# Kernel tuning notes

Hardware: AMD Instinct MI355X
Metric: run time of the kernel (lower is better)

Reference implementation:

```python
import jax, jax.numpy as jnp
import numpy as np

INPUT_DIM = 512
HIDDEN_DIM = 512
B, N = 8, 2048


def setup_inputs() -> dict:
    key = jax.random.key(0)
    ks = jax.random.split(key, 9)
    s_in = 1.0 / np.sqrt(INPUT_DIM)
    s_h = 1.0 / np.sqrt(HIDDEN_DIM)
    return {
        "X": jax.random.normal(ks[0], (B, N, INPUT_DIM), dtype=jnp.float32),
        "Wq": jax.random.uniform(ks[1], (INPUT_DIM, HIDDEN_DIM), minval=-s_in, maxval=s_in),
        "bq": jnp.zeros((HIDDEN_DIM,), jnp.float32),
        "Wk": jax.random.uniform(ks[2], (INPUT_DIM, HIDDEN_DIM), minval=-s_in, maxval=s_in),
        "bk": jnp.zeros((HIDDEN_DIM,), jnp.float32),
        "Wv": jax.random.uniform(ks[3], (INPUT_DIM, HIDDEN_DIM), minval=-s_in, maxval=s_in),
        "bv": jnp.zeros((HIDDEN_DIM,), jnp.float32),
        "Wo": jax.random.uniform(ks[4], (HIDDEN_DIM, INPUT_DIM), minval=-s_h, maxval=s_h),
        "bo": jnp.zeros((INPUT_DIM,), jnp.float32),
        "ln_gamma": jnp.ones((INPUT_DIM,), jnp.float32),
        "ln_beta": jnp.zeros((INPUT_DIM,), jnp.float32),
    }


def reference(X, Wq, bq, Wk, bk, Wv, bv, Wo, bo, ln_gamma, ln_beta):
    q = X @ Wq + bq                      # [B,N,H]
    k = X @ Wk + bk
    v = X @ Wv + bv
    scores = jnp.einsum('bnh,bmh->bnm', q, k) / jnp.sqrt(jnp.float32(HIDDEN_DIM))
    attn = jax.nn.softmax(scores, axis=-1)      # [B,N,N]
    ctx = jnp.einsum('bnm,bmh->bnh', attn, v)   # [B,N,H]
    out = ctx @ Wo + bo + X                      # residual
    mu = jnp.mean(out, axis=-1, keepdims=True)
    var = jnp.var(out, axis=-1, keepdims=True)
    normed = (out - mu) / jnp.sqrt(var + 1e-5)
    return normed * ln_gamma + ln_beta
```

## Files before the change

### kernel.cpp

```cpp
#include <hip/hip_runtime.h>
#include <cstdint>
#include <cstddef>


typedef __bf16 bf16x8 __attribute__((ext_vector_type(8)));
typedef float  f32x4  __attribute__((ext_vector_type(4)));

__device__ __forceinline__ uint16_t f2bf(float f) {
  union { float f; uint32_t u; } v; v.f = f;
  uint32_t r = v.u + 0x7FFFu + ((v.u >> 16) & 1u);
  return (uint16_t)(r >> 16);
}

__device__ __forceinline__ void gld16(const uint16_t* g, uint16_t* l) {
  __builtin_amdgcn_global_load_lds(
      (__attribute__((address_space(1))) void*)(g),
      (__attribute__((address_space(3))) void*)(l), 16, 0, 0);
}

template <int MODE, int BM, int BN, int WM, int WN>
__global__ __launch_bounds__(512, 4) void gemm_k(
    const uint16_t* __restrict__ A, const uint16_t* __restrict__ Bt,
    void* __restrict__ OutA, uint16_t* __restrict__ OutK,
    uint16_t* __restrict__ OutVT, float* __restrict__ rsum, int K, int lda,
    int ldb, const float* __restrict__ b0, const float* __restrict__ b1,
    const float* __restrict__ b2, const float* __restrict__ Xres, float scale) {
  constexpr int MT = (BM / WM) / 16;
  constexpr int NT = (BN / WN) / 16;
  static_assert(MT == 4 && NT == 4, "wave tile must be 64x64");
  constexpr int AI = (BM >= 128) ? BM / 128 : 1;
  constexpr int BI = BN / 128;
  constexpr int PW = AI + BI;
  __shared__ alignas(16) uint16_t As[3][BM * 32];
  __shared__ alignas(16) uint16_t Bs[3][BN * 32];

  const int tid = threadIdx.x;
  const int w = tid >> 6, lane = tid & 63;
  const int wm = w / WN, wn = w % WN;

  const int gx = gridDim.x, gy = gridDim.y;
  const int nwg = gx * gy * gridDim.z;
  const int hw = blockIdx.x + gx * (blockIdx.y + gy * blockIdx.z);
  const int lg = (hw & 7) * (nwg >> 3) + (hw >> 3);
  const int bx = lg % gx, byz = lg / gx;
  const int by = byz % gy, z = byz / gy;

  const int m0 = by * BM, n0 = bx * BN;

  const uint16_t* Ab = A;
  const uint16_t* Bb = Bt;
  if (MODE == 1) { Ab += (size_t)z * 2048 * 512;  Bb += (size_t)z * 2048 * 512; }
  if (MODE == 2) { Ab += (size_t)z * 2048 * 2048; Bb += (size_t)z * 512 * 2048; }

  const int kc = (((lane & 3) ^ ((lane >> 2) & 3) ^ (lane >> 4)) * 8);
  const int rbA = (BM >= 128) ? w * (BM / 8) : (w & 3) * 16;
  const int rbB = w * (BN / 8);
  const uint16_t* gA = Ab + (size_t)(m0 + rbA + (lane >> 2)) * lda + kc;
  const uint16_t* gB = Bb + (size_t)(n0 + rbB + (lane >> 2)) * ldb + kc;

  f32x4 acc[MT][NT];
#pragma unroll
  for (int i = 0; i < MT; i++)
#pragma unroll
    for (int j = 0; j < NT; j++) acc[i][j] = (f32x4){0.f, 0.f, 0.f, 0.f};

  const int lr = lane & 15, q4 = lane >> 4;
  const int swz = (((lane >> 4) ^ (lr & 3) ^ (lr >> 2)) * 8);
  const int iters = K >> 5;

  auto stage = [&](int t, int buf) {
    const int k0 = t * 32;
#pragma unroll
    for (int j = 0; j < AI; j++)
      gld16(gA + k0 + (size_t)(j * 16) * lda, &As[buf][(rbA + j * 16) * 32]);
#pragma unroll
    for (int j = 0; j < BI; j++)
      gld16(gB + k0 + (size_t)(j * 16) * ldb, &Bs[buf][(rbB + j * 16) * 32]);
  };

  auto compute = [&](int buf) {
    bf16x8 af[MT], bfr[NT];
#pragma unroll
    for (int t = 0; t < MT; t++)
      af[t] = *(const bf16x8*)&As[buf][(wm * (BM / WM) + t * 16 + lr) * 32 + swz];
#pragma unroll
    for (int t = 0; t < NT; t++)
      bfr[t] = *(const bf16x8*)&Bs[buf][(wn * (BN / WN) + t * 16 + lr) * 32 + swz];
#pragma unroll
    for (int nt = 0; nt < NT; nt++)
#pragma unroll
      for (int mt = 0; mt < MT; mt++)
        acc[mt][nt] = __builtin_amdgcn_mfma_f32_16x16x32_bf16(
            af[mt], bfr[nt], acc[mt][nt], 0, 0, 0);
  };

  stage(0, 0);
  stage(1, 1);
  int buf = 0;
  for (int i = 0; i < iters - 1; ++i) {
    asm volatile("s_waitcnt vmcnt(%0)" ::"i"(PW) : "memory");
    __builtin_amdgcn_s_barrier();
    if (i + 2 < iters) stage(i + 2, (buf + 2 >= 3) ? buf - 1 : buf + 2);
    compute(buf);
    buf = (buf == 2) ? 0 : buf + 1;
  }
  asm volatile("s_waitcnt vmcnt(0)" ::: "memory");
  __builtin_amdgcn_s_barrier();
  compute(buf);

  if (MODE == 1) {
    uint16_t* Sp = (uint16_t*)OutA + (size_t)z * 2048 * 2048;
#pragma unroll
    for (int mt = 0; mt < MT; mt++) {
      float rp[4] = {0.f, 0.f, 0.f, 0.f};
#pragma unroll
      for (int nt = 0; nt < NT; nt++) {
#pragma unroll
        for (int i = 0; i < 4; i++) {
          const int row = m0 + wm * (BM / WM) + mt * 16 + q4 * 4 + i;
          const int col = n0 + wn * (BN / WN) + nt * 16 + lr;
          const float e = __expf(acc[mt][nt][i] * scale);
          Sp[(size_t)row * 2048 + col] = f2bf(e);
          rp[i] += e;
        }
      }
#pragma unroll
      for (int i = 0; i < 4; i++) {
        float p = rp[i];
        p += __shfl_xor(p, 1); p += __shfl_xor(p, 2);
        p += __shfl_xor(p, 4); p += __shfl_xor(p, 8);
        if (lr == 0) {
          const int row = m0 + wm * (BM / WM) + mt * 16 + q4 * 4 + i;
          atomicAdd(&rsum[z * 2048 + row], p);
        }
      }
    }
  } else if (MODE == 2) {
#pragma unroll
    for (int mt = 0; mt < MT; mt++) {
#pragma unroll
      for (int i = 0; i < 4; i++) {
        const int row = m0 + wm * (BM / WM) + mt * 16 + q4 * 4 + i;
        const float sc = 1.0f / rsum[z * 2048 + row];
#pragma unroll
        for (int nt = 0; nt < NT; nt++) {
          const int col = n0 + wn * (BN / WN) + nt * 16 + lr;
          ((uint16_t*)OutA)[((size_t)z * 2048 + row) * 512 + col] =
              f2bf(acc[mt][nt][i] * sc);
        }
      }
    }
  } else if (MODE == 4) {
    __shared__ float redS[8][64];
    __shared__ float redQ[8][64];
    float* Op = (float*)OutA;
    __syncthreads();
#pragma unroll
    for (int mt = 0; mt < MT; mt++) {
#pragma unroll
      for (int i = 0; i < 4; i++) {
        const int rl = mt * 16 + q4 * 4 + i;
        const int row = m0 + rl;
        float ps = 0.f, pq = 0.f;
#pragma unroll
        for (int nt = 0; nt < NT; nt++) {
          const int col = wn * 64 + nt * 16 + lr;
          float v = acc[mt][nt][i] + b0[col] + Xres[(size_t)row * 512 + col];
          acc[mt][nt][i] = v;
          ps += v; pq += v * v;
        }
        ps += __shfl_xor(ps, 1); pq += __shfl_xor(pq, 1);
        ps += __shfl_xor(ps, 2); pq += __shfl_xor(pq, 2);
        ps += __shfl_xor(ps, 4); pq += __shfl_xor(pq, 4);
        ps += __shfl_xor(ps, 8); pq += __shfl_xor(pq, 8);
        if (lr == 0) { redS[w][rl] = ps; redQ[w][rl] = pq; }
      }
    }
    __syncthreads();
#pragma unroll
    for (int mt = 0; mt < MT; mt++) {
#pragma unroll
      for (int i = 0; i < 4; i++) {
        const int rl = mt * 16 + q4 * 4 + i;
        const int row = m0 + rl;
        float s8 = 0.f, q8 = 0.f;
#pragma unroll
        for (int ww = 0; ww < 8; ww++) { s8 += redS[ww][rl]; q8 += redQ[ww][rl]; }
        const float mean = s8 * (1.f / 512.f);
        const float var = q8 * (1.f / 512.f) - mean * mean;
        const float rstd = rsqrtf(var + 1e-5f);
#pragma unroll
        for (int nt = 0; nt < NT; nt++) {
          const int col = wn * 64 + nt * 16 + lr;
          Op[(size_t)row * 512 + col] =
              (acc[mt][nt][i] - mean) * rstd * b1[col] + b2[col];
        }
      }
    }
  } else {
#pragma unroll
    for (int mt = 0; mt < MT; mt++) {
#pragma unroll
      for (int nt = 0; nt < NT; nt++) {
#pragma unroll
        for (int i = 0; i < 4; i++) {
          const int row = m0 + wm * (BM / WM) + mt * 16 + q4 * 4 + i;
          const int col = n0 + wn * (BN / WN) + nt * 16 + lr;
          const float v = acc[mt][nt][i];
          const int which = col >> 9, c = col & 511;
          if (which == 0) {
            ((uint16_t*)OutA)[(size_t)row * 512 + c] = f2bf(v + b0[c]);
          } else if (which == 1) {
            OutK[(size_t)row * 512 + c] = f2bf(v + b1[c]);
          } else {
            OutVT[(size_t)(row >> 11) * (512 * 2048) + (size_t)c * 2048 +
                  (row & 2047)] = f2bf(v + b2[c]);
          }
        }
      }
    }
  }
}

__global__ __launch_bounds__(256) void cvt_all_k(
    const float* __restrict__ X, uint16_t* __restrict__ Xb,
    const float* __restrict__ Wq, const float* __restrict__ Wk,
    const float* __restrict__ Wv, const float* __restrict__ Wo,
    uint16_t* __restrict__ Wt, float* __restrict__ rsum) {
  const int i = blockIdx.x * 256 + threadIdx.x;
  const float4 f = ((const float4*)X)[i];
  uint32_t lo = (uint32_t)f2bf(f.x) | ((uint32_t)f2bf(f.y) << 16);
  uint32_t hi = (uint32_t)f2bf(f.z) | ((uint32_t)f2bf(f.w) << 16);
  ((uint2*)Xb)[i] = make_uint2(lo, hi);
  if (i < 16384) rsum[i] = 0.f;
  if (i < 2048 * 512) {
    const int n = i >> 9, kk = i & 511;
    const int which = n >> 9, c = n & 511;
    const float* W =
        (which == 0) ? Wq : (which == 1) ? Wk : (which == 2) ? Wv : Wo;
    Wt[i] = f2bf(W[kk * 512 + c]);
  }
}

extern "C" void kernel_launch(void* const* d_in, const int* in_sizes, int n_in,
                              void* d_out, int out_size, void* d_ws,
                              size_t ws_size, hipStream_t stream) {
  const float* X     = (const float*)d_in[0];
  const float* Wq    = (const float*)d_in[1];
  const float* bq    = (const float*)d_in[2];
  const float* Wk    = (const float*)d_in[3];
  const float* bk    = (const float*)d_in[4];
  const float* Wv    = (const float*)d_in[5];
  const float* bv    = (const float*)d_in[6];
  const float* Wo    = (const float*)d_in[7];
  const float* bo    = (const float*)d_in[8];
  const float* gamma = (const float*)d_in[9];
  const float* beta  = (const float*)d_in[10];
  float* out = (float*)d_out;

  char* ws = (char*)d_ws;
  uint16_t* S    = (uint16_t*)(ws);
  uint16_t* Xb   = (uint16_t*)(ws);
  uint16_t* Wt   = (uint16_t*)(ws + 67108864);
  uint16_t* q    = (uint16_t*)(ws + 69206016);
  uint16_t* kb   = (uint16_t*)(ws + 85983232);
  uint16_t* vT   = (uint16_t*)(ws + 102760448);
  float*    rsum = (float*)(ws + 119537664);
  uint16_t* ctx  = q;

  cvt_all_k<<<dim3(8192), dim3(256), 0, stream>>>(X, Xb, Wq, Wk, Wv, Wo, Wt,
                                                  rsum);
  gemm_k<0, 256, 128, 4, 2><<<dim3(12, 64, 1), dim3(512), 0, stream>>>(
      Xb, Wt, (void*)q, kb, vT, nullptr, 512, 512, 512, bq, bk, bv, nullptr,
      1.f);
  gemm_k<1, 256, 128, 4, 2><<<dim3(16, 8, 8), dim3(512), 0, stream>>>(
      q, kb, (void*)S, nullptr, nullptr, rsum, 512, 512, 512, nullptr, nullptr,
      nullptr, nullptr, 0.044194173824159216f);
  gemm_k<2, 256, 128, 4, 2><<<dim3(4, 8, 8), dim3(512), 0, stream>>>(
      S, vT, (void*)ctx, nullptr, nullptr, rsum, 2048, 2048, 2048, nullptr,
      nullptr, nullptr, nullptr, 1.f);
  gemm_k<4, 64, 512, 1, 8><<<dim3(1, 256, 1), dim3(512), 0, stream>>>(
      ctx, Wt + 1536 * 512, (void*)out, nullptr, nullptr, nullptr, 512, 512,
      512, bo, gamma, beta, X, 1.f);
}
```

Measured before the change: 316.8 us.

## Add BK=64 double-buffered GEMM kernel with 256-wide tiles for QKV/attention

```diff
diff --git a/kernel.cpp b/kernel.cpp
--- a/kernel.cpp
+++ b/kernel.cpp
@@ -18,25 +18,24 @@
       (__attribute__((address_space(3))) void*)(l), 16, 0, 0);
 }
 
-template <int MODE, int BM, int BN, int WM, int WN>
-__global__ __launch_bounds__(512, 4) void gemm_k(
+template <int MODE, int BM, int BN>
+__global__ __launch_bounds__(512, 2) void gemm2_k(
     const uint16_t* __restrict__ A, const uint16_t* __restrict__ Bt,
     void* __restrict__ OutA, uint16_t* __restrict__ OutK,
     uint16_t* __restrict__ OutVT, float* __restrict__ rsum, int K, int lda,
     int ldb, const float* __restrict__ b0, const float* __restrict__ b1,
-    const float* __restrict__ b2, const float* __restrict__ Xres, float scale) {
-  constexpr int MT = (BM / WM) / 16;
-  constexpr int NT = (BN / WN) / 16;
-  static_assert(MT == 4 && NT == 4, "wave tile must be 64x64");
-  constexpr int AI = (BM >= 128) ? BM / 128 : 1;
-  constexpr int BI = BN / 128;
-  constexpr int PW = AI + BI;
-  __shared__ alignas(16) uint16_t As[3][BM * 32];
-  __shared__ alignas(16) uint16_t Bs[3][BN * 32];
+    const float* __restrict__ b2, float scale) {
+  constexpr int MT = (BM / 2) / 16;
+  constexpr int NT = (BN / 4) / 16;
+  constexpr int AI = BM / 64;
+  constexpr int BI = BN / 64;
+  static_assert(NT == 4, "BN must be 256");
+  __shared__ alignas(16) uint16_t As[2][BM * 64];
+  __shared__ alignas(16) uint16_t Bs[2][BN * 64];
 
   const int tid = threadIdx.x;
   const int w = tid >> 6, lane = tid & 63;
-  const int wm = w / WN, wn = w % WN;
+  const int wm = w >> 2, wn = w & 3;
 
   const int gx = gridDim.x, gy = gridDim.y;
   const int nwg = gx * gy * gridDim.z;
@@ -52,11 +51,22 @@
   if (MODE == 1) { Ab += (size_t)z * 2048 * 512;  Bb += (size_t)z * 2048 * 512; }
   if (MODE == 2) { Ab += (size_t)z * 2048 * 2048; Bb += (size_t)z * 512 * 2048; }
 
-  const int kc = (((lane & 3) ^ ((lane >> 2) & 3) ^ (lane >> 4)) * 8);
-  const int rbA = (BM >= 128) ? w * (BM / 8) : (w & 3) * 16;
-  const int rbB = w * (BN / 8);
-  const uint16_t* gA = Ab + (size_t)(m0 + rbA + (lane >> 2)) * lda + kc;
-  const uint16_t* gB = Bb + (size_t)(n0 + rbB + (lane >> 2)) * ldb + kc;
+  const int l3 = lane >> 3, l7 = lane & 7;
+  const int csw = (l7 ^ l3) * 8;
+  const uint16_t* gA = Ab + (size_t)(m0 + w * (BM / 8) + l3) * lda + csw;
+  const uint16_t* gB = Bb + (size_t)(n0 + w * (BN / 8) + l3) * ldb + csw;
+
+  auto stage = [&](int t, int b) {
+    const int k0 = t * 64;
+#pragma unroll
+    for (int j = 0; j < AI; j++)
+      gld16(gA + k0 + (size_t)(j * 8) * lda,
+            &As[b][(w * (BM / 8) + j * 8) * 64]);
+#pragma unroll
+    for (int j = 0; j < BI; j++)
+      gld16(gB + k0 + (size_t)(j * 8) * ldb,
+            &Bs[b][(w * (BN / 8) + j * 8) * 64]);
+  };
 
   f32x4 acc[MT][NT];
 #pragma unroll
@@ -65,48 +75,43 @@
     for (int j = 0; j < NT; j++) acc[i][j] = (f32x4){0.f, 0.f, 0.f, 0.f};
 
   const int lr = lane & 15, q4 = lane >> 4;
-  const int swz = (((lane >> 4) ^ (lr & 3) ^ (lr >> 2)) * 8);
-  const int iters = K >> 5;
-
-  auto stage = [&](int t, int buf) {
-    const int k0 = t * 32;
-#pragma unroll
-    for (int j = 0; j < AI; j++)
-      gld16(gA + k0 + (size_t)(j * 16) * lda, &As[buf][(rbA + j * 16) * 32]);
-#pragma unroll
-    for (int j = 0; j < BI; j++)
-      gld16(gB + k0 + (size_t)(j * 16) * ldb, &Bs[buf][(rbB + j * 16) * 32]);
-  };
-
-  auto compute = [&](int buf) {
-    bf16x8 af[MT], bfr[NT];
-#pragma unroll
-    for (int t = 0; t < MT; t++)
-      af[t] = *(const bf16x8*)&As[buf][(wm * (BM / WM) + t * 16 + lr) * 32 + swz];
-#pragma unroll
-    for (int t = 0; t < NT; t++)
-      bfr[t] = *(const bf16x8*)&Bs[buf][(wn * (BN / WN) + t * 16 + lr) * 32 + swz];
-#pragma unroll
-    for (int nt = 0; nt < NT; nt++)
-#pragma unroll
-      for (int mt = 0; mt < MT; mt++)
-        acc[mt][nt] = __builtin_amdgcn_mfma_f32_16x16x32_bf16(
-            af[mt], bfr[nt], acc[mt][nt], 0, 0, 0);
-  };
+  const int rc0 = ((q4) ^ (lr & 7)) * 8;
+  const int rc1 = ((4 + q4) ^ (lr & 7)) * 8;
+
+  const int NK = K >> 6;
 
   stage(0, 0);
-  stage(1, 1);
-  int buf = 0;
-  for (int i = 0; i < iters - 1; ++i) {
-    asm volatile("s_waitcnt vmcnt(%0)" ::"i"(PW) : "memory");
-    __builtin_amdgcn_s_barrier();
-    if (i + 2 < iters) stage(i + 2, (buf + 2 >= 3) ? buf - 1 : buf + 2);
-    compute(buf);
-    buf = (buf == 2) ? 0 : buf + 1;
-  }
   asm volatile("s_waitcnt vmcnt(0)" ::: "memory");
   __builtin_amdgcn_s_barrier();
-  compute(buf);
+
+  int cur = 0;
+  for (int t = 0; t < NK; ++t) {
+    if (t + 1 < NK) stage(t + 1, cur ^ 1);
+#pragma unroll
+    for (int ks = 0; ks < 2; ks++) {
+      const int rc = ks ? rc1 : rc0;
+      bf16x8 af[MT], bfr[NT];
+#pragma unroll
+      for (int mt = 0; mt < MT; mt++)
+        af[mt] = *(const bf16x8*)
+            &As[cur][(wm * (BM / 2) + mt * 16 + lr) * 64 + rc];
+#pragma unroll
+      for (int nt = 0; nt < NT; nt++)
+        bfr[nt] = *(const bf16x8*)&Bs[cur][(wn * 64 + nt * 16 + lr) * 64 + rc];
+#pragma unroll
+      for (int nt = 0; nt < NT; nt++)
+#pragma unroll
+        for (int mt = 0; mt < MT; mt++)
+          acc[mt][nt] = __builtin_amdgcn_mfma_f32_16x16x32_bf16(
+              af[mt], bfr[nt], acc[mt][nt], 0, 0, 0);
+    }
+    if (t + 1 < NK) {
+      asm volatile("s_waitcnt lgkmcnt(0)" ::: "memory");
+      asm volatile("s_waitcnt vmcnt(0)" ::: "memory");
+      __builtin_amdgcn_s_barrier();
+      cur ^= 1;
+    }
+  }
 
   if (MODE == 1) {
     uint16_t* Sp = (uint16_t*)OutA + (size_t)z * 2048 * 2048;
@@ -117,8 +122,8 @@
       for (int nt = 0; nt < NT; nt++) {
 #pragma unroll
         for (int i = 0; i < 4; i++) {
-          const int row = m0 + wm * (BM / WM) + mt * 16 + q4 * 4 + i;
-          const int col = n0 + wn * (BN / WN) + nt * 16 + lr;
+          const int row = m0 + wm * (BM / 2) + mt * 16 + q4 * 4 + i;
+          const int col = n0 + wn * 64 + nt * 16 + lr;
           const float e = __expf(acc[mt][nt][i] * scale);
           Sp[(size_t)row * 2048 + col] = f2bf(e);
           rp[i] += e;
@@ -130,7 +135,7 @@
         p += __shfl_xor(p, 1); p += __shfl_xor(p, 2);
         p += __shfl_xor(p, 4); p += __shfl_xor(p, 8);
         if (lr == 0) {
-          const int row = m0 + wm * (BM / WM) + mt * 16 + q4 * 4 + i;
+          const int row = m0 + wm * (BM / 2) + mt * 16 + q4 * 4 + i;
           atomicAdd(&rsum[z * 2048 + row], p);
         }
       }
@@ -140,72 +145,25 @@
     for (int mt = 0; mt < MT; mt++) {
 #pragma unroll
       for (int i = 0; i < 4; i++) {
-        const int row = m0 + wm * (BM / WM) + mt * 16 + q4 * 4 + i;
+        const int row = m0 + wm * (BM / 2) + mt * 16 + q4 * 4 + i;
         const float sc = 1.0f / rsum[z * 2048 + row];
 #pragma unroll
         for (int nt = 0; nt < NT; nt++) {
-          const int col = n0 + wn * (BN / WN) + nt * 16 + lr;
+          const int col = n0 + wn * 64 + nt * 16 + lr;
           ((uint16_t*)OutA)[((size_t)z * 2048 + row) * 512 + col] =
               f2bf(acc[mt][nt][i] * sc);
         }
       }
     }
-  } else if (MODE == 4) {
-    __shared__ float redS[8][64];
-    __shared__ float redQ[8][64];
-    float* Op = (float*)OutA;
-    __syncthreads();
+  } else {
 #pragma unroll
     for (int mt = 0; mt < MT; mt++) {
 #pragma unroll
-      for (int i = 0; i < 4; i++) {
-        const int rl = mt * 16 + q4 * 4 + i;
-        const int row = m0 + rl;
-        float ps = 0.f, pq = 0.f;
-#pragma unroll
-        for (int nt = 0; nt < NT; nt++) {
-          const int col = wn * 64 + nt * 16 + lr;
-          float v = acc[mt][nt][i] + b0[col] + Xres[(size_t)row * 512 + col];
-          acc[mt][nt][i] = v;
-          ps += v; pq += v * v;
-        }
-        ps += __shfl_xor(ps, 1); pq += __shfl_xor(pq, 1);
-        ps += __shfl_xor(ps, 2); pq += __shfl_xor(pq, 2);
-        ps += __shfl_xor(ps, 4); pq += __shfl_xor(pq, 4);
-        ps += __shfl_xor(ps, 8); pq += __shfl_xor(pq, 8);
-        if (lr == 0) { redS[w][rl] = ps; redQ[w][rl] = pq; }
-      }
-    }
-    __syncthreads();
-#pragma unroll
-    for (int mt = 0; mt < MT; mt++) {
-#pragma unroll
-      for (int i = 0; i < 4; i++) {
-        const int rl = mt * 16 + q4 * 4 + i;
-        const int row = m0 + rl;
-        float s8 = 0.f, q8 = 0.f;
-#pragma unroll
-        for (int ww = 0; ww < 8; ww++) { s8 += redS[ww][rl]; q8 += redQ[ww][rl]; }
-        const float mean = s8 * (1.f / 512.f);
-        const float var = q8 * (1.f / 512.f) - mean * mean;
-        const float rstd = rsqrtf(var + 1e-5f);
-#pragma unroll
-        for (int nt = 0; nt < NT; nt++) {
-          const int col = wn * 64 + nt * 16 + lr;
-          Op[(size_t)row * 512 + col] =
-              (acc[mt][nt][i] - mean) * rstd * b1[col] + b2[col];
-        }
-      }
-    }
-  } else {
-#pragma unroll
-    for (int mt = 0; mt < MT; mt++) {
-#pragma unroll
       for (int nt = 0; nt < NT; nt++) {
 #pragma unroll
         for (int i = 0; i < 4; i++) {
-          const int row = m0 + wm * (BM / WM) + mt * 16 + q4 * 4 + i;
-          const int col = n0 + wn * (BN / WN) + nt * 16 + lr;
+          const int row = m0 + wm * (BM / 2) + mt * 16 + q4 * 4 + i;
+          const int col = n0 + wn * 64 + nt * 16 + lr;
           const float v = acc[mt][nt][i];
           const int which = col >> 9, c = col & 511;
           if (which == 0) {
@@ -217,6 +175,141 @@
                   (row & 2047)] = f2bf(v + b2[c]);
           }
         }
+      }
+    }
+  }
+}
+
+template <int MODE, int BM, int BN, int WM, int WN>
+__global__ __launch_bounds__(512, 4) void gemm_k(
+    const uint16_t* __restrict__ A, const uint16_t* __restrict__ Bt,
+    void* __restrict__ OutA, float* __restrict__ rsum, int K, int lda,
+    int ldb, const float* __restrict__ b0, const float* __restrict__ b1,
+    const float* __restrict__ b2, const float* __restrict__ Xres) {
+  constexpr int MT = (BM / WM) / 16;
+  constexpr int NT = (BN / WN) / 16;
+  static_assert(MT == 4 && NT == 4, "wave tile must be 64x64");
+  constexpr int AI = (BM >= 128) ? BM / 128 : 1;
+  constexpr int BI = BN / 128;
+  constexpr int PW = AI + BI;
+  __shared__ alignas(16) uint16_t As[3][BM * 32];
+  __shared__ alignas(16) uint16_t Bs[3][BN * 32];
+
+  const int tid = threadIdx.x;
+  const int w = tid >> 6, lane = tid & 63;
+  const int wm = w / WN, wn = w % WN;
+
+  const int gx = gridDim.x, gy = gridDim.y;
+  const int nwg = gx * gy * gridDim.z;
+  const int hw = blockIdx.x + gx * (blockIdx.y + gy * blockIdx.z);
+  const int lg = (hw & 7) * (nwg >> 3) + (hw >> 3);
+  const int bx = lg % gx, byz = lg / gx;
+  const int by = byz % gy;
+
+  const int m0 = by * BM, n0 = bx * BN;
+
+  const uint16_t* Ab = A;
+  const uint16_t* Bb = Bt;
+
+  const int kc = (((lane & 3) ^ ((lane >> 2) & 3) ^ (lane >> 4)) * 8);
+  const int rbA = (BM >= 128) ? w * (BM / 8) : (w & 3) * 16;
+  const int rbB = w * (BN / 8);
+  const uint16_t* gA = Ab + (size_t)(m0 + rbA + (lane >> 2)) * lda + kc;
+  const uint16_t* gB = Bb + (size_t)(n0 + rbB + (lane >> 2)) * ldb + kc;
+
+  f32x4 acc[MT][NT];
+#pragma unroll
+  for (int i = 0; i < MT; i++)
+#pragma unroll
+    for (int j = 0; j < NT; j++) acc[i][j] = (f32x4){0.f, 0.f, 0.f, 0.f};
+
+  const int lr = lane & 15, q4 = lane >> 4;
+  const int swz = (((lane >> 4) ^ (lr & 3) ^ (lr >> 2)) * 8);
+  const int iters = K >> 5;
+
+  auto stage = [&](int t, int buf) {
+    const int k0 = t * 32;
+#pragma unroll
+    for (int j = 0; j < AI; j++)
+      gld16(gA + k0 + (size_t)(j * 16) * lda, &As[buf][(rbA + j * 16) * 32]);
+#pragma unroll
+    for (int j = 0; j < BI; j++)
+      gld16(gB + k0 + (size_t)(j * 16) * ldb, &Bs[buf][(rbB + j * 16) * 32]);
+  };
+
+  auto compute = [&](int buf) {
+    bf16x8 af[MT], bfr[NT];
+#pragma unroll
+    for (int t = 0; t < MT; t++)
+      af[t] = *(const bf16x8*)&As[buf][(wm * (BM / WM) + t * 16 + lr) * 32 + swz];
+#pragma unroll
+    for (int t = 0; t < NT; t++)
+      bfr[t] = *(const bf16x8*)&Bs[buf][(wn * (BN / WN) + t * 16 + lr) * 32 + swz];
+#pragma unroll
+    for (int nt = 0; nt < NT; nt++)
+#pragma unroll
+      for (int mt = 0; mt < MT; mt++)
+        acc[mt][nt] = __builtin_amdgcn_mfma_f32_16x16x32_bf16(
+            af[mt], bfr[nt], acc[mt][nt], 0, 0, 0);
+  };
+
+  stage(0, 0);
+  stage(1, 1);
+  int buf = 0;
+  for (int i = 0; i < iters - 1; ++i) {
+    asm volatile("s_waitcnt vmcnt(%0)" ::"i"(PW) : "memory");
+    __builtin_amdgcn_s_barrier();
+    if (i + 2 < iters) stage(i + 2, (buf + 2 >= 3) ? buf - 1 : buf + 2);
+    compute(buf);
+    buf = (buf == 2) ? 0 : buf + 1;
+  }
+  asm volatile("s_waitcnt vmcnt(0)" ::: "memory");
+  __builtin_amdgcn_s_barrier();
+  compute(buf);
+
+  __shared__ float redS[8][64];
+  __shared__ float redQ[8][64];
+  float* Op = (float*)OutA;
+  __syncthreads();
+#pragma unroll
+  for (int mt = 0; mt < MT; mt++) {
+#pragma unroll
+    for (int i = 0; i < 4; i++) {
+      const int rl = mt * 16 + q4 * 4 + i;
+      const int row = m0 + rl;
+      float ps = 0.f, pq = 0.f;
+#pragma unroll
+      for (int nt = 0; nt < NT; nt++) {
+        const int col = wn * 64 + nt * 16 + lr;
+        float v = acc[mt][nt][i] + b0[col] + Xres[(size_t)row * 512 + col];
+        acc[mt][nt][i] = v;
+        ps += v; pq += v * v;
+      }
+      ps += __shfl_xor(ps, 1); pq += __shfl_xor(pq, 1);
+      ps += __shfl_xor(ps, 2); pq += __shfl_xor(pq, 2);
+      ps += __shfl_xor(ps, 4); pq += __shfl_xor(pq, 4);
+      ps += __shfl_xor(ps, 8); pq += __shfl_xor(pq, 8);
+      if (lr == 0) { redS[w][rl] = ps; redQ[w][rl] = pq; }
+    }
+  }
+  __syncthreads();
+#pragma unroll
+  for (int mt = 0; mt < MT; mt++) {
+#pragma unroll
+    for (int i = 0; i < 4; i++) {
+      const int rl = mt * 16 + q4 * 4 + i;
+      const int row = m0 + rl;
+      float s8 = 0.f, q8 = 0.f;
+#pragma unroll
+      for (int ww = 0; ww < 8; ww++) { s8 += redS[ww][rl]; q8 += redQ[ww][rl]; }
+      const float mean = s8 * (1.f / 512.f);
+      const float var = q8 * (1.f / 512.f) - mean * mean;
+      const float rstd = rsqrtf(var + 1e-5f);
+#pragma unroll
+      for (int nt = 0; nt < NT; nt++) {
+        const int col = wn * 64 + nt * 16 + lr;
+        Op[(size_t)row * 512 + col] =
+            (acc[mt][nt][i] - mean) * rstd * b1[col] + b2[col];
       }
     }
   }
@@ -270,16 +363,15 @@
 
   cvt_all_k<<<dim3(8192), dim3(256), 0, stream>>>(X, Xb, Wq, Wk, Wv, Wo, Wt,
                                                   rsum);
-  gemm_k<0, 256, 128, 4, 2><<<dim3(12, 64, 1), dim3(512), 0, stream>>>(
-      Xb, Wt, (void*)q, kb, vT, nullptr, 512, 512, 512, bq, bk, bv, nullptr,
-      1.f);
-  gemm_k<1, 256, 128, 4, 2><<<dim3(16, 8, 8), dim3(512), 0, stream>>>(
+  gemm2_k<0, 256, 256><<<dim3(6, 64, 1), dim3(512), 0, stream>>>(
+      Xb, Wt, (void*)q, kb, vT, nullptr, 512, 512, 512, bq, bk, bv, 1.f);
+  gemm2_k<1, 256, 256><<<dim3(8, 8, 8), dim3(512), 0, stream>>>(
       q, kb, (void*)S, nullptr, nullptr, rsum, 512, 512, 512, nullptr, nullptr,
-      nullptr, nullptr, 0.044194173824159216f);
-  gemm_k<2, 256, 128, 4, 2><<<dim3(4, 8, 8), dim3(512), 0, stream>>>(
+      nullptr, 0.044194173824159216f);
+  gemm2_k<2, 128, 256><<<dim3(2, 16, 8), dim3(512), 0, stream>>>(
       S, vT, (void*)ctx, nullptr, nullptr, rsum, 2048, 2048, 2048, nullptr,
-      nullptr, nullptr, nullptr, 1.f);
+      nullptr, nullptr, 1.f);
   gemm_k<4, 64, 512, 1, 8><<<dim3(1, 256, 1), dim3(512), 0, stream>>>(
-      ctx, Wt + 1536 * 512, (void*)out, nullptr, nullptr, nullptr, 512, 512,
-      512, bo, gamma, beta, X, 1.f);
-}
+      ctx, Wt + 1536 * 512, (void*)out, nullptr, 512, 512, 512, bo, gamma,
+      beta, X);
+}
```

Result: slower. 338.2 us (+6.8%).
